# Kernel optimization log

Measured on AMD Instinct MI355X. Metric: run time of the kernel, lower is better.

Reference implementation:

```python
import jax, jax.numpy as jnp
import numpy as np

B, T, N, H = 256, 128, 1024, 1024


def setup_inputs() -> dict:
    key = jax.random.key(0)
    ks = jax.random.split(key, 7)
    s = 0.05
    return {
        "input_data": jax.random.normal(ks[0], (B, T, N), jnp.float32),
        "W_ih": jax.random.normal(ks[1], (4 * H, N), jnp.float32) * s,
        "W_hh": jax.random.normal(ks[2], (4 * H, H), jnp.float32) * s,
        "b_ih": jax.random.normal(ks[3], (4 * H,), jnp.float32) * s,
        "b_hh": jax.random.normal(ks[4], (4 * H,), jnp.float32) * s,
        "attn_w": jax.random.normal(ks[5], (2 * H + T,), jnp.float32) * s,
        "attn_b": jax.random.normal(ks[6], (1,), jnp.float32) * s,
    }


def reference(input_data, W_ih, W_hh, b_ih, b_hh, attn_w, attn_b):
    # input_data: [B, T, N]; torch LSTM gate order i, f, g, o.
    Bsz, Tn, Nn = input_data.shape
    Hn = W_hh.shape[1]
    # Decompose the attn linear over the concat [h, c, x_hist]:
    # score = h @ w_h + c @ w_c + x_perm @ w_x + b  (exactly the original Linear)
    w_h, w_c, w_x = attn_w[:Hn], attn_w[Hn:2 * Hn], attn_w[2 * Hn:]
    x_perm = jnp.transpose(input_data, (0, 2, 1))            # [B, N, T]
    score_x = x_perm @ w_x + attn_b[0]                        # [B, N], constant over t

    def step(carry, x_t):
        h, c = carry                                          # [B, H] each
        score = (h @ w_h + c @ w_c)[:, None] + score_x        # [B, N]
        a = jax.nn.softmax(score, axis=1)                     # [B, N]
        w_in = a * x_t                                        # weighted input [B, N]
        gates = w_in @ W_ih.T + b_ih + h @ W_hh.T + b_hh      # [B, 4H]
        i, f, g, o = jnp.split(gates, 4, axis=1)
        c_new = jax.nn.sigmoid(f) * c + jax.nn.sigmoid(i) * jnp.tanh(g)
        h_new = jax.nn.sigmoid(o) * jnp.tanh(c_new)
        return (h_new, c_new), (w_in, h_new)

    h0 = jnp.zeros((Bsz, Hn), input_data.dtype)
    c0 = jnp.zeros((Bsz, Hn), input_data.dtype)
    xs = jnp.transpose(input_data, (1, 0, 2))                 # [T, B, N]
    _, (iw, ie) = jax.lax.scan(step, (h0, c0), xs)
    input_weighted = jnp.transpose(iw, (1, 0, 2))             # [B, T, N]
    input_encoded = jnp.transpose(ie, (1, 0, 2))              # [B, T, H]
    return input_weighted, input_encoded
```

## Files before the change

### kernel.cpp

```cpp
#include <hip/hip_runtime.h>
#include <hip/hip_bf16.h>

#define BB 256
#define TT 128
#define NN 1024
#define HH 1024
#define G4 4096

typedef __attribute__((ext_vector_type(4))) float f32x4;
typedef __attribute__((ext_vector_type(8))) short bf16x8;

__device__ __forceinline__ unsigned short f2bf(float f) {
    unsigned int u = __builtin_bit_cast(unsigned int, f);
    u += 0x7FFFu + ((u >> 16) & 1u);
    return (unsigned short)(u >> 16);
}
__device__ __forceinline__ float bf2f(unsigned short s) {
    unsigned int u = ((unsigned int)s) << 16;
    return __builtin_bit_cast(float, u);
}

__global__ __launch_bounds__(512) void k_attn(
    const float* __restrict__ x, const float* __restrict__ attn_w,
    const float* __restrict__ attn_b, float* __restrict__ out0,
    unsigned short* __restrict__ win_bf)
{
    const int b = blockIdx.x;
    const int tid = threadIdx.x;
    const float* xb = x + (size_t)b * (TT * NN);
    const float* wx = attn_w + 2 * HH;

    float s0 = 0.f, s1 = 0.f;
    for (int t = 0; t < TT; ++t) {
        float2 v = *(const float2*)(xb + (size_t)t * NN + tid * 2);
        float w = wx[t];
        s0 += v.x * w; s1 += v.y * w;
    }
    float ab = attn_b[0];
    s0 += ab; s1 += ab;

    __shared__ float red[8];
    const int wv = tid >> 6, ln = tid & 63;
    float m = fmaxf(s0, s1);
#pragma unroll
    for (int off = 32; off > 0; off >>= 1) m = fmaxf(m, __shfl_xor(m, off));
    if (ln == 0) red[wv] = m;
    __syncthreads();
    m = red[0];
#pragma unroll
    for (int i = 1; i < 8; ++i) m = fmaxf(m, red[i]);

    float e0 = expf(s0 - m), e1 = expf(s1 - m);
    float sum = e0 + e1;
#pragma unroll
    for (int off = 32; off > 0; off >>= 1) sum += __shfl_xor(sum, off);
    __syncthreads();
    if (ln == 0) red[wv] = sum;
    __syncthreads();
    sum = 0.f;
#pragma unroll
    for (int i = 0; i < 8; ++i) sum += red[i];
    const float inv = 1.0f / sum;
    const float a0 = e0 * inv, a1 = e1 * inv;

    float* o = out0 + (size_t)b * (TT * NN);
    unsigned short* wb = win_bf + (size_t)b * (TT * NN);
    for (int t = 0; t < TT; ++t) {
        float2 v = *(const float2*)(xb + (size_t)t * NN + tid * 2);
        float2 w; w.x = a0 * v.x; w.y = a1 * v.y;
        *(float2*)(o + (size_t)t * NN + tid * 2) = w;
        unsigned int pk = (unsigned int)f2bf(w.x) | ((unsigned int)f2bf(w.y) << 16);
        *(unsigned int*)(wb + (size_t)t * NN + tid * 2) = pk;
    }
}

__global__ __launch_bounds__(256) void k_prep_w(
    const float* __restrict__ Wih, const float* __restrict__ Whh,
    const float* __restrict__ bih, const float* __restrict__ bhh,
    unsigned short* __restrict__ WihP, unsigned short* __restrict__ WhhP,
    float* __restrict__ biasP)
{
    const int p = blockIdx.x;
    const int j = p >> 2, g = p & 3;
    const int r = g * HH + j;
    const int tid = threadIdx.x;
    {
        float4 v = *(const float4*)(Wih + (size_t)r * NN + tid * 4);
        ushort4 o;
        o.x = f2bf(v.x); o.y = f2bf(v.y); o.z = f2bf(v.z); o.w = f2bf(v.w);
        *(ushort4*)(WihP + (size_t)p * NN + tid * 4) = o;
    }
    {
        float4 v = *(const float4*)(Whh + (size_t)r * HH + tid * 4);
        ushort4 o;
        o.x = f2bf(v.x); o.y = f2bf(v.y); o.z = f2bf(v.z); o.w = f2bf(v.w);
        *(ushort4*)(WhhP + (size_t)p * HH + tid * 4) = o;
    }
    if (tid == 0) biasP[p] = bih[r] + bhh[r];
}

__global__ __launch_bounds__(256) void k_gemm_xp(
    const unsigned short* __restrict__ A,
    const unsigned short* __restrict__ Bm,
    unsigned short* __restrict__ C)
{
    __shared__ unsigned short lA[128 * 32];
    __shared__ unsigned short lB[128 * 32];

    const int bid = blockIdx.x;
    const int cpx = gridDim.x >> 3;
    const int swz = (bid & 7) * cpx + (bid >> 3);
    const int NTN = G4 / 128;
    const int tm = swz / NTN, tn = swz % NTN;

    const int tid = threadIdx.x;
    const int wv = tid >> 6, ln = tid & 63;
    const int wr = wv >> 1, wc = wv & 1;

    f32x4 acc[4][4] = {};

    const unsigned short* Ag = A + (size_t)tm * 128 * NN;
    const unsigned short* Bg = Bm + (size_t)tn * 128 * NN;
    const int srow = ln >> 2;
    const int sseg = ln & 3;

    for (int k0 = 0; k0 < NN; k0 += 32) {
        __syncthreads();
#pragma unroll
        for (int q = 0; q < 2; ++q) {
            const int row = wv * 32 + q * 16 + srow;
            __builtin_amdgcn_global_load_lds(
                (const __attribute__((address_space(1))) void*)(Ag + (size_t)row * NN + k0 + sseg * 8),
                (__attribute__((address_space(3))) void*)(&lA[(wv * 32 + q * 16) * 32]),
                16, 0, 0);
            __builtin_amdgcn_global_load_lds(
                (const __attribute__((address_space(1))) void*)(Bg + (size_t)row * NN + k0 + sseg * 8),
                (__attribute__((address_space(3))) void*)(&lB[(wv * 32 + q * 16) * 32]),
                16, 0, 0);
        }
        __syncthreads();

        const int rlo = ln & 15, khi = ln >> 4;
        bf16x8 af[4], bfr[4];
#pragma unroll
        for (int m = 0; m < 4; ++m)
            af[m] = *(const bf16x8*)&lA[(wr * 64 + m * 16 + rlo) * 32 + khi * 8];
#pragma unroll
        for (int n = 0; n < 4; ++n)
            bfr[n] = *(const bf16x8*)&lB[(wc * 64 + n * 16 + rlo) * 32 + khi * 8];
#pragma unroll
        for (int m = 0; m < 4; ++m)
#pragma unroll
            for (int n = 0; n < 4; ++n)
                acc[m][n] = __builtin_amdgcn_mfma_f32_16x16x32_bf16(af[m], bfr[n], acc[m][n], 0, 0, 0);
    }

    const int rlo = ln & 15, rhi = ln >> 4;
#pragma unroll
    for (int m = 0; m < 4; ++m)
#pragma unroll
        for (int n = 0; n < 4; ++n)
#pragma unroll
            for (int j = 0; j < 4; ++j) {
                const int row = tm * 128 + wr * 64 + m * 16 + rhi * 4 + j;
                const int col = tn * 128 + wc * 64 + n * 16 + rlo;
                C[(size_t)row * G4 + col] = f2bf(acc[m][n][j]);
            }
}

__global__ __launch_bounds__(512) void k_step3(
    const int t,
    const unsigned short* __restrict__ hbf,
    const unsigned short* __restrict__ WhhP,
    const unsigned short* __restrict__ Xp,
    const float* __restrict__ biasP,
    float* __restrict__ cbuf,
    unsigned short* __restrict__ hbf_out,
    float* __restrict__ out1)
{
    __shared__ unsigned short lA[3][64 * 128];
    __shared__ unsigned short lB[3][64 * 128];
    __shared__ unsigned short lXp[64 * 64];

    const int bid = blockIdx.x;
    const int ti = bid >> 6, tj = bid & 63;
    const int tid = threadIdx.x;
    const int wv = tid >> 6, ln = tid & 63;
    const int wr = wv >> 1, wc = wv & 1;
    const int rlo = ln & 15, khi = ln >> 4;

    {
        const size_t bg = (size_t)(ti * 64 + wv * 8 + (ln >> 3));
        __builtin_amdgcn_global_load_lds(
            (const __attribute__((address_space(1))) void*)((const char*)Xp + ((bg * TT + t) << 13) + tj * 128 + (ln & 7) * 16),
            (__attribute__((address_space(3))) void*)((char*)lXp + wv * 1024),
            16, 0, 0);
    }

    const char* Ab = (const char*)hbf + (size_t)(ti * 64) * 2048;
    const char* Bb = (const char*)WhhP + (size_t)(tj * 64) * 2048;

#define STAGE(buf_, c_) do { \
    _Pragma("unroll") \
    for (int q_ = 0; q_ < 2; ++q_) { \
        const int r_ = q_ * 32 + wv * 4 + (ln >> 4); \
        const int so_ = (((ln & 15) ^ (r_ & 7)) << 4); \
        __builtin_amdgcn_global_load_lds( \
            (const __attribute__((address_space(1))) void*)(Ab + (size_t)r_ * 2048 + (c_) * 256 + so_), \
            (__attribute__((address_space(3))) void*)((char*)&lA[buf_][0] + q_ * 8192 + wv * 1024), \
            16, 0, 0); \
        __builtin_amdgcn_global_load_lds( \
            (const __attribute__((address_space(1))) void*)(Bb + (size_t)r_ * 2048 + (c_) * 256 + so_), \
            (__attribute__((address_space(3))) void*)((char*)&lB[buf_][0] + q_ * 8192 + wv * 1024), \
            16, 0, 0); \
    } } while (0)

    STAGE(0, 0);
    STAGE(1, 1);
    STAGE(2, 2);

    float4 bias4[2];
#pragma unroll
    for (int n = 0; n < 2; ++n)
        bias4[n] = *(const float4*)&biasP[(tj * 16 + wc * 8 + n * 4 + ((ln & 15) >> 2)) * 4];

    f32x4 acc[2] = {};

#pragma unroll
    for (int c = 0; c < 8; ++c) {
        const int buf = c % 3;
        if (c < 6)       { asm volatile("s_waitcnt vmcnt(8)" ::: "memory"); }
        else if (c == 6) { asm volatile("s_waitcnt vmcnt(4)" ::: "memory"); }
        else             { asm volatile("s_waitcnt vmcnt(0)" ::: "memory"); }
        __builtin_amdgcn_s_barrier();

        bf16x8 af[4], bfr[4][2];
#pragma unroll
        for (int kk = 0; kk < 4; ++kk) {
            {
                const int row = wr * 16 + rlo;
                const int off = (kk * 64 + khi * 16) ^ ((row & 7) << 4);
                af[kk] = *(const bf16x8*)((const char*)&lA[buf][0] + row * 256 + off);
            }
#pragma unroll
            for (int n = 0; n < 2; ++n) {
                const int row = wc * 32 + n * 16 + rlo;
                const int off = (kk * 64 + khi * 16) ^ ((row & 7) << 4);
                bfr[kk][n] = *(const bf16x8*)((const char*)&lB[buf][0] + row * 256 + off);
            }
        }
        asm volatile("s_waitcnt lgkmcnt(0)" ::: "memory");
        __builtin_amdgcn_sched_barrier(0);
        __builtin_amdgcn_s_barrier();
        if (c < 5) STAGE((c + 3) % 3, c + 3);
#pragma unroll
        for (int kk = 0; kk < 4; ++kk)
#pragma unroll
            for (int n = 0; n < 2; ++n)
                acc[n] = __builtin_amdgcn_mfma_f32_16x16x32_bf16(af[kk], bfr[kk][n], acc[n], 0, 0, 0);
    }
#undef STAGE

#pragma unroll
    for (int n = 0; n < 2; ++n) {
        f32x4 v = acc[n], u, w;
#pragma unroll
        for (int k = 0; k < 4; ++k) {
            float s = __shfl_xor(v[k ^ 1], 1);
            u[k] = ((k & 1) == (ln & 1)) ? v[k] : s;
        }
#pragma unroll
        for (int k = 0; k < 4; ++k) {
            float s = __shfl_xor(u[k ^ 2], 2);
            w[k] = (((k >> 1) & 1) == ((ln >> 1) & 1)) ? u[k] : s;
        }
        const int r_loc = wr * 16 + ((ln >> 4) << 2) + (ln & 3);
        const int u_loc = wc * 8 + n * 4 + ((ln & 15) >> 2);
        const ushort4 xp4 = *(const ushort4*)((const char*)lXp + r_loc * 128 + u_loc * 8);
        const float gi = w[0] + bf2f(xp4.x) + bias4[n].x;
        const float gf = w[1] + bf2f(xp4.y) + bias4[n].y;
        const float gg = w[2] + bf2f(xp4.z) + bias4[n].z;
        const float go = w[3] + bf2f(xp4.w) + bias4[n].w;
        const float i_ = 1.f / (1.f + expf(-gi));
        const float f_ = 1.f / (1.f + expf(-gf));
        const float g_ = tanhf(gg);
        const float o_ = 1.f / (1.f + expf(-go));
        const int bg = ti * 64 + r_loc;
        const int ug = tj * 16 + u_loc;
        const float cprev = cbuf[(size_t)bg * HH + ug];
        const float cc = f_ * cprev + i_ * g_;
        cbuf[(size_t)bg * HH + ug] = cc;
        const float h_ = o_ * tanhf(cc);
        out1[(size_t)bg * (TT * HH) + (size_t)t * HH + ug] = h_;
        hbf_out[(size_t)bg * HH + ug] = f2bf(h_);
    }
}

__global__ __launch_bounds__(256) void k_zero(float4* __restrict__ p)
{
    p[blockIdx.x * 256 + threadIdx.x] = make_float4(0.f, 0.f, 0.f, 0.f);
}

extern "C" void kernel_launch(void* const* d_in, const int* in_sizes, int n_in,
                              void* d_out, int out_size, void* d_ws, size_t ws_size,
                              hipStream_t stream)
{
    const float* x      = (const float*)d_in[0];
    const float* Wih    = (const float*)d_in[1];
    const float* Whh    = (const float*)d_in[2];
    const float* bih    = (const float*)d_in[3];
    const float* bhh    = (const float*)d_in[4];
    const float* attn_w = (const float*)d_in[5];
    const float* attn_b = (const float*)d_in[6];

    float* out0 = (float*)d_out;
    float* out1 = (float*)d_out + (size_t)BB * TT * NN;

    char* w = (char*)d_ws;
    unsigned short* WihP  = (unsigned short*)(w);
    unsigned short* WhhP  = (unsigned short*)(w + 8388608);
    float*          biasP = (float*)(w + 16777216);
    unsigned short* winbf = (unsigned short*)(w + 16793600);
    unsigned short* Xp    = (unsigned short*)(w + 83902464);
    unsigned short* hbf0  = (unsigned short*)(w + 352337920);
    unsigned short* hbf1  = (unsigned short*)(w + 352862208);
    float*          cbuf  = (float*)(w + 353386496);

    k_attn<<<BB, 512, 0, stream>>>(x, attn_w, attn_b, out0, winbf);
    k_prep_w<<<G4, 256, 0, stream>>>(Wih, Whh, bih, bhh, WihP, WhhP, biasP);
    k_gemm_xp<<<(BB * TT / 128) * (G4 / 128), 256, 0, stream>>>(winbf, WihP, Xp);
    k_zero<<<512, 256, 0, stream>>>((float4*)hbf0);

    for (int t = 0; t < TT; ++t) {
        const unsigned short* hin = (t & 1) ? hbf1 : hbf0;
        unsigned short* hout      = (t & 1) ? hbf0 : hbf1;
        k_step3<<<256, 512, 0, stream>>>(t, hin, WhhP, Xp, biasP, cbuf, hout, out1);
    }
}
```

Before: 1.717 ms.

## Load h operand directly into registers instead of staging through LDS

The recurrent step kernel now reads each wave's full slice of the h (A) operand for the whole K dimension straight into registers (32 bf16x8 fragments) at the start, instead of staging it through a triple-buffered LDS pipeline. Only the W_hh (B) operand still goes through LDS, so the vmcnt wait thresholds are halved. The Xp gate preactivations are also loaded directly into registers rather than via LDS. This cuts LDS traffic and footprint and removes the LDS reads of A. In exchange it adds many vector registers, which may lower occupancy or cause spills, and the A reads from global memory are uncoalesced and duplicated across waves.

```diff
diff --git a/kernel.cpp b/kernel.cpp
--- a/kernel.cpp
+++ b/kernel.cpp
@@ -168,7 +168,7 @@
             }
 }
 
-__global__ __launch_bounds__(512) void k_step3(
+__global__ __launch_bounds__(512) void k_step6(
     const int t,
     const unsigned short* __restrict__ hbf,
     const unsigned short* __restrict__ WhhP,
@@ -178,9 +178,7 @@
     unsigned short* __restrict__ hbf_out,
     float* __restrict__ out1)
 {
-    __shared__ unsigned short lA[3][64 * 128];
     __shared__ unsigned short lB[3][64 * 128];
-    __shared__ unsigned short lXp[64 * 64];
 
     const int bid = blockIdx.x;
     const int ti = bid >> 6, tj = bid & 63;
@@ -189,15 +187,31 @@
     const int wr = wv >> 1, wc = wv & 1;
     const int rlo = ln & 15, khi = ln >> 4;
 
-    {
-        const size_t bg = (size_t)(ti * 64 + wv * 8 + (ln >> 3));
-        __builtin_amdgcn_global_load_lds(
-            (const __attribute__((address_space(1))) void*)((const char*)Xp + ((bg * TT + t) << 13) + tj * 128 + (ln & 7) * 16),
-            (__attribute__((address_space(3))) void*)((char*)lXp + wv * 1024),
-            16, 0, 0);
-    }
-
-    const char* Ab = (const char*)hbf + (size_t)(ti * 64) * 2048;
+    const int r_loc = wr * 16 + ((ln >> 4) << 2) + (ln & 3);
+    const int u_loc0 = wc * 8 + ((ln & 15) >> 2);
+    const int bg = ti * 64 + r_loc;
+
+    ushort4 xp4[2];
+#pragma unroll
+    for (int n = 0; n < 2; ++n)
+        xp4[n] = *(const ushort4*)((const char*)Xp +
+                    ((size_t)bg * TT + t) * 8192 + tj * 128 + (u_loc0 + n * 4) * 8);
+
+    float4 bias4[2];
+#pragma unroll
+    for (int n = 0; n < 2; ++n)
+        bias4[n] = *(const float4*)&biasP[(tj * 16 + u_loc0 + n * 4) * 4];
+
+    const char* arow = (const char*)hbf + (size_t)(ti * 64 + wr * 16 + rlo) * 2048 + khi * 16;
+    bf16x8 afr[8][4];
+#pragma unroll
+    for (int c = 0; c < 8; ++c)
+#pragma unroll
+        for (int kk = 0; kk < 4; ++kk)
+            afr[c][kk] = *(const bf16x8*)(arow + c * 256 + kk * 64);
+
+    __builtin_amdgcn_sched_barrier(0);
+
     const char* Bb = (const char*)WhhP + (size_t)(tj * 64) * 2048;
 
 #define STAGE(buf_, c_) do { \
@@ -206,10 +220,6 @@
         const int r_ = q_ * 32 + wv * 4 + (ln >> 4); \
         const int so_ = (((ln & 15) ^ (r_ & 7)) << 4); \
         __builtin_amdgcn_global_load_lds( \
-            (const __attribute__((address_space(1))) void*)(Ab + (size_t)r_ * 2048 + (c_) * 256 + so_), \
-            (__attribute__((address_space(3))) void*)((char*)&lA[buf_][0] + q_ * 8192 + wv * 1024), \
-            16, 0, 0); \
-        __builtin_amdgcn_global_load_lds( \
             (const __attribute__((address_space(1))) void*)(Bb + (size_t)r_ * 2048 + (c_) * 256 + so_), \
             (__attribute__((address_space(3))) void*)((char*)&lB[buf_][0] + q_ * 8192 + wv * 1024), \
             16, 0, 0); \
@@ -219,36 +229,25 @@
     STAGE(1, 1);
     STAGE(2, 2);
 
-    float4 bias4[2];
-#pragma unroll
-    for (int n = 0; n < 2; ++n)
-        bias4[n] = *(const float4*)&biasP[(tj * 16 + wc * 8 + n * 4 + ((ln & 15) >> 2)) * 4];
-
     f32x4 acc[2] = {};
 
 #pragma unroll
     for (int c = 0; c < 8; ++c) {
         const int buf = c % 3;
-        if (c < 6)       { asm volatile("s_waitcnt vmcnt(8)" ::: "memory"); }
-        else if (c == 6) { asm volatile("s_waitcnt vmcnt(4)" ::: "memory"); }
+        if (c < 6)       { asm volatile("s_waitcnt vmcnt(4)" ::: "memory"); }
+        else if (c == 6) { asm volatile("s_waitcnt vmcnt(2)" ::: "memory"); }
         else             { asm volatile("s_waitcnt vmcnt(0)" ::: "memory"); }
         __builtin_amdgcn_s_barrier();
 
-        bf16x8 af[4], bfr[4][2];
-#pragma unroll
-        for (int kk = 0; kk < 4; ++kk) {
-            {
-                const int row = wr * 16 + rlo;
-                const int off = (kk * 64 + khi * 16) ^ ((row & 7) << 4);
-                af[kk] = *(const bf16x8*)((const char*)&lA[buf][0] + row * 256 + off);
-            }
+        bf16x8 bfr[4][2];
+#pragma unroll
+        for (int kk = 0; kk < 4; ++kk)
 #pragma unroll
             for (int n = 0; n < 2; ++n) {
                 const int row = wc * 32 + n * 16 + rlo;
                 const int off = (kk * 64 + khi * 16) ^ ((row & 7) << 4);
                 bfr[kk][n] = *(const bf16x8*)((const char*)&lB[buf][0] + row * 256 + off);
             }
-        }
         asm volatile("s_waitcnt lgkmcnt(0)" ::: "memory");
         __builtin_amdgcn_sched_barrier(0);
         __builtin_amdgcn_s_barrier();
@@ -257,7 +256,7 @@
         for (int kk = 0; kk < 4; ++kk)
 #pragma unroll
             for (int n = 0; n < 2; ++n)
-                acc[n] = __builtin_amdgcn_mfma_f32_16x16x32_bf16(af[kk], bfr[kk][n], acc[n], 0, 0, 0);
+                acc[n] = __builtin_amdgcn_mfma_f32_16x16x32_bf16(afr[c][kk], bfr[kk][n], acc[n], 0, 0, 0);
     }
 #undef STAGE
 
@@ -274,19 +273,15 @@
             float s = __shfl_xor(u[k ^ 2], 2);
             w[k] = (((k >> 1) & 1) == ((ln >> 1) & 1)) ? u[k] : s;
         }
-        const int r_loc = wr * 16 + ((ln >> 4) << 2) + (ln & 3);
-        const int u_loc = wc * 8 + n * 4 + ((ln & 15) >> 2);
-        const ushort4 xp4 = *(const ushort4*)((const char*)lXp + r_loc * 128 + u_loc * 8);
-        const float gi = w[0] + bf2f(xp4.x) + bias4[n].x;
-        const float gf = w[1] + bf2f(xp4.y) + bias4[n].y;
-        const float gg = w[2] + bf2f(xp4.z) + bias4[n].z;
-        const float go = w[3] + bf2f(xp4.w) + bias4[n].w;
+        const float gi = w[0] + bf2f(xp4[n].x) + bias4[n].x;
+        const float gf = w[1] + bf2f(xp4[n].y) + bias4[n].y;
+        const float gg = w[2] + bf2f(xp4[n].z) + bias4[n].z;
+        const float go = w[3] + bf2f(xp4[n].w) + bias4[n].w;
         const float i_ = 1.f / (1.f + expf(-gi));
         const float f_ = 1.f / (1.f + expf(-gf));
         const float g_ = tanhf(gg);
         const float o_ = 1.f / (1.f + expf(-go));
-        const int bg = ti * 64 + r_loc;
-        const int ug = tj * 16 + u_loc;
+        const int ug = tj * 16 + u_loc0 + n * 4;
         const float cprev = cbuf[(size_t)bg * HH + ug];
         const float cc = f_ * cprev + i_ * g_;
         cbuf[(size_t)bg * HH + ug] = cc;
@@ -334,6 +329,6 @@
     for (int t = 0; t < TT; ++t) {
         const unsigned short* hin = (t & 1) ? hbf1 : hbf0;
         unsigned short* hout      = (t & 1) ? hbf0 : hbf1;
-        k_step3<<<256, 512, 0, stream>>>(t, hin, WhhP, Xp, biasP, cbuf, hout, out1);
-    }
-}
+        k_step6<<<256, 512, 0, stream>>>(t, hin, WhhP, Xp, biasP, cbuf, hout, out1);
+    }
+}
```

Measured after the change: 2.445 ms. 42.4% more time.
